# Performance work log

Measured on AMD Instinct MI355X. Metric: run time of the kernel, lower is better.

## Reference

```python
import jax, jax.numpy as jnp
import numpy as np

EPS = 1e-05
ITERS = 3


def safe_norm(s, axis):
    return jnp.sqrt(jnp.sum(s * s, axis=axis, keepdims=True) + EPS)


def squash(s, axis):
    norm = safe_norm(s, axis)
    return (norm / (1.0 + norm)) * s / norm


def setup_inputs() -> dict:
    key = jax.random.key(0)
    k1, k2 = jax.random.split(key)
    b, B, C, P, h, w = 4, 288, 32, 16, 14, 14  # B = K*K*32, P = pose 4x4
    u = jax.random.normal(k1, (b, B, C, P, h, w), dtype=jnp.float32)
    a = jax.random.uniform(k2, (b, B, h, w), dtype=jnp.float32)
    return {"u": u, "a": a}


def reference(u, a):
    # mode='dynamic': activation a is unused by this routing variant.
    # max_min_norm over pose axis (3), max/min over input-capsule axis (1)
    norm = safe_norm(u, 3)                          # (b,B,C,1,h,w)
    max_n = jnp.max(norm, axis=1, keepdims=True)    # (b,1,C,1,h,w)
    min_n = jnp.min(norm, axis=1, keepdims=True)
    u = u / (max_n - min_n)

    b, B, C, P, h, w = u.shape
    r = jnp.zeros((b, B, C, 1, h, w), dtype=u.dtype)
    v = None
    for i in range(ITERS):
        c = jax.nn.softmax(r, axis=2)                               # over C
        v = squash(jnp.sum(c * u, axis=1, keepdims=True), 3)        # (b,1,C,P,h,w)
        if i != ITERS - 1:
            r = r + jnp.sum(u * v, axis=3, keepdims=True)           # agreement
    a_out = safe_norm(v, 3)                                         # (b,1,C,1,h,w)
    return (jnp.squeeze(v, 1), jnp.squeeze(jnp.squeeze(a_out, 1), 2))
```

## Files before the change

### kernel.cpp

```cpp
#include <hip/hip_runtime.h>


constexpr int kB    = 4;
constexpr int kIC   = 288;
constexpr int kOC   = 32;
constexpr int kP    = 16;
constexpr int kHW   = 196;
constexpr int kNPOS = kB * kHW;
constexpr int kPAIR = 16;
constexpr int kNTILES = 25;
constexpr int kNCH  = 16;
constexpr int kBCH  = kIC / kNCH;
constexpr int kSCP  = kOC * kP * kNPOS;
constexpr int kSC   = kOC * kNPOS;
constexpr int kBStride2 = kOC * kP * kHW / 2;
constexpr int kNBLK = kNTILES * kNCH;
constexpr float kEPS = 1e-5f;

__device__ inline void decomp(int l, int& tile, int& chunk) {
    const int logical = (l & 7) * (kNBLK / 8) + (l >> 3);
    tile  = logical >> 4;
    chunk = logical & 15;
}

__global__ __launch_bounds__(512, 4) void pass1_kernel(
    const float* __restrict__ U, float* __restrict__ s0,
    unsigned int* __restrict__ maxb, unsigned int* __restrict__ minb)
{
    int tile, chunk;
    decomp(blockIdx.x, tile, chunk);
    const int tid = threadIdx.x;
    const int j   = tid & 15;
    const int c   = tid >> 4;
    int n0 = tile * 32 + 2 * j;
    const bool valid = (n0 < kNPOS);
    if (!valid) n0 = kNPOS - 2;
    const int b  = n0 / kHW;
    const int hw = n0 - b * kHW;
    const int B0 = chunk * kBCH;
    const float2* up = (const float2*)(U + (size_t)(((b * kIC + B0) * kOC + c) * kP) * kHW + hw);

    float2 sacc[kP];
#pragma unroll
    for (int p = 0; p < kP; ++p) sacc[p] = make_float2(0.f, 0.f);
    float2 mx = make_float2(0.f, 0.f);
    float2 mn = make_float2(3.4e38f, 3.4e38f);

    for (int Bi = 0; Bi < kBCH; ++Bi) {
        float2 u[kP];
#pragma unroll
        for (int p = 0; p < kP; ++p) u[p] = up[p * (kHW / 2)];
        float2 nsq = make_float2(kEPS, kEPS);
#pragma unroll
        for (int p = 0; p < kP; ++p) {
            nsq.x = fmaf(u[p].x, u[p].x, nsq.x);
            nsq.y = fmaf(u[p].y, u[p].y, nsq.y);
            sacc[p].x += u[p].x;
            sacc[p].y += u[p].y;
        }
        const float nrx = sqrtf(nsq.x), nry = sqrtf(nsq.y);
        mx.x = fmaxf(mx.x, nrx); mx.y = fmaxf(mx.y, nry);
        mn.x = fminf(mn.x, nrx); mn.y = fminf(mn.y, nry);
        up += kBStride2;
    }
    if (valid) {
        const int cn = c * kNPOS + n0;
        atomicMax(&maxb[cn],     __float_as_uint(mx.x));
        atomicMax(&maxb[cn + 1], __float_as_uint(mx.y));
        atomicMin(&minb[cn],     __float_as_uint(mn.x));
        atomicMin(&minb[cn + 1], __float_as_uint(mn.y));
#pragma unroll
        for (int p = 0; p < kP; ++p) {
            atomicAdd(&s0[(c * kP + p) * kNPOS + n0],     sacc[p].x);
            atomicAdd(&s0[(c * kP + p) * kNPOS + n0 + 1], sacc[p].y);
        }
    }
}

__global__ void v0_kernel(float* __restrict__ s0,
                          const unsigned int* __restrict__ maxb,
                          const unsigned int* __restrict__ minb,
                          float* __restrict__ scaleb)
{
    const int i = blockIdx.x * blockDim.x + threadIdx.x;
    if (i >= kSC) return;
    const int c = i / kNPOS;
    const int n = i - c * kNPOS;
    const float mx = __uint_as_float(maxb[i]);
    const float mn = __uint_as_float(minb[i]);
    const float sc = 1.f / (mx - mn);
    scaleb[i] = sc;
    float sv[kP];
    float nsq = kEPS;
#pragma unroll
    for (int p = 0; p < kP; ++p) {
        const float v = s0[(c * kP + p) * kNPOS + n] * sc * (1.f / 32.f);
        sv[p] = v;
        nsq = fmaf(v, v, nsq);
    }
    const float inv = 1.f / (1.f + sqrtf(nsq));
#pragma unroll
    for (int p = 0; p < kP; ++p)
        s0[(c * kP + p) * kNPOS + n] = sv[p] * inv;
}

__global__ __launch_bounds__(512, 3) void route_kernel(
    const float* __restrict__ U, const float* __restrict__ Vr,
    const float* __restrict__ scaleb, float* __restrict__ sout)
{
    __shared__ float2 ldsM[8 * kPAIR];
    __shared__ float2 ldsS[8 * kPAIR];
    int tile, chunk;
    decomp(blockIdx.x, tile, chunk);
    const int tid = threadIdx.x;
    const int j   = tid & 15;
    const int c   = tid >> 4;
    const int wv  = tid >> 6;
    int n0 = tile * 32 + 2 * j;
    const bool valid = (n0 < kNPOS);
    if (!valid) n0 = kNPOS - 2;
    const int b  = n0 / kHW;
    const int hw = n0 - b * kHW;
    const int B0 = chunk * kBCH;
    const float2* up = (const float2*)(U + (size_t)(((b * kIC + B0) * kOC + c) * kP) * kHW + hw);

    float2 vr[kP];
#pragma unroll
    for (int p = 0; p < kP; ++p)
        vr[p] = *(const float2*)&Vr[(c * kP + p) * kNPOS + n0];
    const float2 sc = *(const float2*)&scaleb[c * kNPOS + n0];

    float2 acc[kP];
#pragma unroll
    for (int p = 0; p < kP; ++p) acc[p] = make_float2(0.f, 0.f);

    for (int Bi = 0; Bi < kBCH; ++Bi) {
        float2 u[kP];
#pragma unroll
        for (int p = 0; p < kP; ++p) u[p] = up[p * (kHW / 2)];
        float2 d = make_float2(0.f, 0.f);
#pragma unroll
        for (int p = 0; p < kP; ++p) {
            d.x = fmaf(u[p].x, vr[p].x, d.x);
            d.y = fmaf(u[p].y, vr[p].y, d.y);
        }
        float2 r = make_float2(sc.x * d.x, sc.y * d.y);

        float2 m = r;
        m.x = fmaxf(m.x, __shfl_xor(m.x, 16)); m.y = fmaxf(m.y, __shfl_xor(m.y, 16));
        m.x = fmaxf(m.x, __shfl_xor(m.x, 32)); m.y = fmaxf(m.y, __shfl_xor(m.y, 32));
        if ((tid & 63) < kPAIR) ldsM[wv * kPAIR + j] = m;
        __syncthreads();
        float2 mxv = ldsM[j];
#pragma unroll
        for (int w = 1; w < 8; ++w) {
            const float2 t = ldsM[w * kPAIR + j];
            mxv.x = fmaxf(mxv.x, t.x); mxv.y = fmaxf(mxv.y, t.y);
        }
        const float2 e = make_float2(__expf(r.x - mxv.x), __expf(r.y - mxv.y));
        float2 z = e;
        z.x += __shfl_xor(z.x, 16); z.y += __shfl_xor(z.y, 16);
        z.x += __shfl_xor(z.x, 32); z.y += __shfl_xor(z.y, 32);
        if ((tid & 63) < kPAIR) ldsS[wv * kPAIR + j] = z;
        __syncthreads();
        float2 Z = ldsS[j];
#pragma unroll
        for (int w = 1; w < 8; ++w) {
            const float2 t = ldsS[w * kPAIR + j];
            Z.x += t.x; Z.y += t.y;
        }
        const float2 cb = make_float2(e.x / Z.x, e.y / Z.y);
#pragma unroll
        for (int p = 0; p < kP; ++p) {
            acc[p].x = fmaf(cb.x, u[p].x, acc[p].x);
            acc[p].y = fmaf(cb.y, u[p].y, acc[p].y);
        }
        up += kBStride2;
    }
    if (valid) {
#pragma unroll
        for (int p = 0; p < kP; ++p) {
            atomicAdd(&sout[(c * kP + p) * kNPOS + n0],     sc.x * acc[p].x);
            atomicAdd(&sout[(c * kP + p) * kNPOS + n0 + 1], sc.y * acc[p].y);
        }
    }
}

__global__ void v1_kernel(float* __restrict__ v0buf,
                          const float* __restrict__ s1)
{
    const int i = blockIdx.x * blockDim.x + threadIdx.x;
    if (i >= kSC) return;
    const int c = i / kNPOS;
    const int n = i - c * kNPOS;
    float sv[kP];
    float nsq = kEPS;
#pragma unroll
    for (int p = 0; p < kP; ++p) {
        const float v = s1[(c * kP + p) * kNPOS + n];
        sv[p] = v;
        nsq = fmaf(v, v, nsq);
    }
    const float inv = 1.f / (1.f + sqrtf(nsq));
#pragma unroll
    for (int p = 0; p < kP; ++p)
        v0buf[(c * kP + p) * kNPOS + n] += sv[p] * inv;
}

__global__ void final_kernel(const float* __restrict__ s2, float* __restrict__ out)
{
    const int i = blockIdx.x * blockDim.x + threadIdx.x;
    if (i >= kSC) return;
    const int c = i / kNPOS;
    const int n = i - c * kNPOS;
    const int b = n / kHW;
    const int hw = n - b * kHW;
    float sv[kP];
    float nsq = kEPS;
#pragma unroll
    for (int p = 0; p < kP; ++p) {
        const float v = s2[(c * kP + p) * kNPOS + n];
        sv[p] = v;
        nsq = fmaf(v, v, nsq);
    }
    const float inv = 1.f / (1.f + sqrtf(nsq));
    float vs = 0.f;
#pragma unroll
    for (int p = 0; p < kP; ++p) {
        const float v = sv[p] * inv;
        out[(size_t)((b * kOC + c) * kP + p) * kHW + hw] = v;
        vs = fmaf(v, v, vs);
    }
    out[(size_t)kSCP + (b * kOC + c) * kHW + hw] = sqrtf(vs + kEPS);
}

extern "C" void kernel_launch(void* const* d_in, const int* in_sizes, int n_in,
                              void* d_out, int out_size, void* d_ws, size_t ws_size,
                              hipStream_t stream) {
    const float* U = (const float*)d_in[0];
    float* out = (float*)d_out;
    float* ws  = (float*)d_ws;

    float* s0 = ws;
    float* s1 = ws + kSCP;
    float* s2 = ws + 2 * kSCP;
    unsigned int* maxb = (unsigned int*)(ws + 3 * kSCP);
    unsigned int* minb = maxb + kSC;
    float* scaleb = (float*)(minb + kSC);

    hipMemsetAsync(s0, 0, (size_t)3 * kSCP * sizeof(float), stream);
    hipMemsetAsync(maxb, 0, (size_t)kSC * sizeof(unsigned int), stream);
    hipMemsetAsync(minb, 0x7F, (size_t)kSC * sizeof(unsigned int), stream);

    pass1_kernel<<<kNBLK, 512, 0, stream>>>(U, s0, maxb, minb);
    v0_kernel<<<(kSC + 255) / 256, 256, 0, stream>>>(s0, maxb, minb, scaleb);
    route_kernel<<<kNBLK, 512, 0, stream>>>(U, s0, scaleb, s1);
    v1_kernel<<<(kSC + 255) / 256, 256, 0, stream>>>(s0, s1);
    route_kernel<<<kNBLK, 512, 0, stream>>>(U, s0, scaleb, s2);
    final_kernel<<<(kSC + 255) / 256, 256, 0, stream>>>(s2, out);
}
```

Measured before the change: 1.048 ms.

## Cache bf16 relayouted copy of U in pass1 for route kernels

Pass1 now writes a bf16-rounded copy of the input capsules, packed per tile and chunk into a contiguous slab layout. Both routing passes read this packed copy instead of re-reading fp32 U with strided access. This halves the bytes read by the routing passes and makes those loads contiguous, at the cost of an extra write in pass1 and bf16 precision in the agreement and weighted sums.

Result: faster. 953.9 us (-8.9%).

```diff
diff --git a/kernel.cpp b/kernel.cpp
--- a/kernel.cpp
+++ b/kernel.cpp
@@ -1,20 +1,20 @@
 #include <hip/hip_runtime.h>
 
 
-constexpr int kB    = 4;
 constexpr int kIC   = 288;
 constexpr int kOC   = 32;
 constexpr int kP    = 16;
 constexpr int kHW   = 196;
-constexpr int kNPOS = kB * kHW;
-constexpr int kPAIR = 16;
-constexpr int kNTILES = 25;
+constexpr int kNPOS = 4 * kHW;
+constexpr int kNT   = 25;
 constexpr int kNCH  = 16;
 constexpr int kBCH  = kIC / kNCH;
 constexpr int kSCP  = kOC * kP * kNPOS;
 constexpr int kSC   = kOC * kNPOS;
-constexpr int kBStride2 = kOC * kP * kHW / 2;
-constexpr int kNBLK = kNTILES * kNCH;
+constexpr int kNBLK = kNT * kNCH;
+constexpr int kUB   = kOC * kP * kHW;
+constexpr int kRslab = kBCH * 8 * kOC * 16;
+constexpr size_t kRBytes = (size_t)kNBLK * kRslab * 8;
 constexpr float kEPS = 1e-5f;
 
 __device__ inline void decomp(int l, int& tile, int& chunk) {
@@ -23,8 +23,13 @@
     chunk = logical & 15;
 }
 
+__device__ inline unsigned bf16rne(float x) {
+    const unsigned u = __float_as_uint(x);
+    return (u + 0x7FFFu + ((u >> 16) & 1u)) >> 16;
+}
+
 __global__ __launch_bounds__(512, 4) void pass1_kernel(
-    const float* __restrict__ U, float* __restrict__ s0,
+    const float* __restrict__ U, uint2* __restrict__ R, float* __restrict__ s0,
     unsigned int* __restrict__ maxb, unsigned int* __restrict__ minb)
 {
     int tile, chunk;
@@ -38,7 +43,8 @@
     const int b  = n0 / kHW;
     const int hw = n0 - b * kHW;
     const int B0 = chunk * kBCH;
-    const float2* up = (const float2*)(U + (size_t)(((b * kIC + B0) * kOC + c) * kP) * kHW + hw);
+    const float* up = U + (size_t)(((b * kIC + B0) * kOC + c) * kP) * kHW + hw;
+    uint2* Rp = R + (size_t)(tile * kNCH + chunk) * kRslab + c * 16 + j;
 
     float2 sacc[kP];
 #pragma unroll
@@ -47,21 +53,23 @@
     float2 mn = make_float2(3.4e38f, 3.4e38f);
 
     for (int Bi = 0; Bi < kBCH; ++Bi) {
-        float2 u[kP];
-#pragma unroll
-        for (int p = 0; p < kP; ++p) u[p] = up[p * (kHW / 2)];
         float2 nsq = make_float2(kEPS, kEPS);
 #pragma unroll
-        for (int p = 0; p < kP; ++p) {
-            nsq.x = fmaf(u[p].x, u[p].x, nsq.x);
-            nsq.y = fmaf(u[p].y, u[p].y, nsq.y);
-            sacc[p].x += u[p].x;
-            sacc[p].y += u[p].y;
+        for (int p2 = 0; p2 < 8; ++p2) {
+            const float2 a0 = *(const float2*)(up + (2 * p2)     * kHW);
+            const float2 a1 = *(const float2*)(up + (2 * p2 + 1) * kHW);
+            nsq.x = fmaf(a0.x, a0.x, nsq.x); nsq.y = fmaf(a0.y, a0.y, nsq.y);
+            nsq.x = fmaf(a1.x, a1.x, nsq.x); nsq.y = fmaf(a1.y, a1.y, nsq.y);
+            sacc[2 * p2].x     += a0.x; sacc[2 * p2].y     += a0.y;
+            sacc[2 * p2 + 1].x += a1.x; sacc[2 * p2 + 1].y += a1.y;
+            Rp[(Bi * 8 + p2) * (kOC * 16)] =
+                make_uint2(bf16rne(a0.x) | (bf16rne(a0.y) << 16),
+                           bf16rne(a1.x) | (bf16rne(a1.y) << 16));
         }
         const float nrx = sqrtf(nsq.x), nry = sqrtf(nsq.y);
         mx.x = fmaxf(mx.x, nrx); mx.y = fmaxf(mx.y, nry);
         mn.x = fminf(mn.x, nrx); mn.y = fminf(mn.y, nry);
-        up += kBStride2;
+        up += kUB;
     }
     if (valid) {
         const int cn = c * kNPOS + n0;
@@ -105,11 +113,11 @@
 }
 
 __global__ __launch_bounds__(512, 3) void route_kernel(
-    const float* __restrict__ U, const float* __restrict__ Vr,
+    const uint2* __restrict__ R, const float* __restrict__ Vr,
     const float* __restrict__ scaleb, float* __restrict__ sout)
 {
-    __shared__ float2 ldsM[8 * kPAIR];
-    __shared__ float2 ldsS[8 * kPAIR];
+    __shared__ float2 ldsM[8 * 16];
+    __shared__ float2 ldsS[8 * 16];
     int tile, chunk;
     decomp(blockIdx.x, tile, chunk);
     const int tid = threadIdx.x;
@@ -119,10 +127,7 @@
     int n0 = tile * 32 + 2 * j;
     const bool valid = (n0 < kNPOS);
     if (!valid) n0 = kNPOS - 2;
-    const int b  = n0 / kHW;
-    const int hw = n0 - b * kHW;
-    const int B0 = chunk * kBCH;
-    const float2* up = (const float2*)(U + (size_t)(((b * kIC + B0) * kOC + c) * kP) * kHW + hw);
+    const uint2* Rp = R + (size_t)(tile * kNCH + chunk) * kRslab + c * 16 + j;
 
     float2 vr[kP];
 #pragma unroll
@@ -137,7 +142,13 @@
     for (int Bi = 0; Bi < kBCH; ++Bi) {
         float2 u[kP];
 #pragma unroll
-        for (int p = 0; p < kP; ++p) u[p] = up[p * (kHW / 2)];
+        for (int p2 = 0; p2 < 8; ++p2) {
+            const uint2 w = Rp[(Bi * 8 + p2) * (kOC * 16)];
+            u[2 * p2].x     = __uint_as_float(w.x << 16);
+            u[2 * p2].y     = __uint_as_float(w.x & 0xFFFF0000u);
+            u[2 * p2 + 1].x = __uint_as_float(w.y << 16);
+            u[2 * p2 + 1].y = __uint_as_float(w.y & 0xFFFF0000u);
+        }
         float2 d = make_float2(0.f, 0.f);
 #pragma unroll
         for (int p = 0; p < kP; ++p) {
@@ -149,24 +160,24 @@
         float2 m = r;
         m.x = fmaxf(m.x, __shfl_xor(m.x, 16)); m.y = fmaxf(m.y, __shfl_xor(m.y, 16));
         m.x = fmaxf(m.x, __shfl_xor(m.x, 32)); m.y = fmaxf(m.y, __shfl_xor(m.y, 32));
-        if ((tid & 63) < kPAIR) ldsM[wv * kPAIR + j] = m;
+        if ((tid & 63) < 16) ldsM[wv * 16 + j] = m;
         __syncthreads();
         float2 mxv = ldsM[j];
 #pragma unroll
         for (int w = 1; w < 8; ++w) {
-            const float2 t = ldsM[w * kPAIR + j];
+            const float2 t = ldsM[w * 16 + j];
             mxv.x = fmaxf(mxv.x, t.x); mxv.y = fmaxf(mxv.y, t.y);
         }
         const float2 e = make_float2(__expf(r.x - mxv.x), __expf(r.y - mxv.y));
         float2 z = e;
         z.x += __shfl_xor(z.x, 16); z.y += __shfl_xor(z.y, 16);
         z.x += __shfl_xor(z.x, 32); z.y += __shfl_xor(z.y, 32);
-        if ((tid & 63) < kPAIR) ldsS[wv * kPAIR + j] = z;
+        if ((tid & 63) < 16) ldsS[wv * 16 + j] = z;
         __syncthreads();
         float2 Z = ldsS[j];
 #pragma unroll
         for (int w = 1; w < 8; ++w) {
-            const float2 t = ldsS[w * kPAIR + j];
+            const float2 t = ldsS[w * 16 + j];
             Z.x += t.x; Z.y += t.y;
         }
         const float2 cb = make_float2(e.x / Z.x, e.y / Z.y);
@@ -175,7 +186,6 @@
             acc[p].x = fmaf(cb.x, u[p].x, acc[p].x);
             acc[p].y = fmaf(cb.y, u[p].y, acc[p].y);
         }
-        up += kBStride2;
     }
     if (valid) {
 #pragma unroll
@@ -239,12 +249,13 @@
                               hipStream_t stream) {
     const float* U = (const float*)d_in[0];
     float* out = (float*)d_out;
-    float* ws  = (float*)d_ws;
-
-    float* s0 = ws;
-    float* s1 = ws + kSCP;
-    float* s2 = ws + 2 * kSCP;
-    unsigned int* maxb = (unsigned int*)(ws + 3 * kSCP);
+    char* wsb  = (char*)d_ws;
+
+    uint2* R   = (uint2*)wsb;
+    float* s0  = (float*)(wsb + kRBytes);
+    float* s1  = s0 + kSCP;
+    float* s2  = s1 + kSCP;
+    unsigned int* maxb = (unsigned int*)(s2 + kSCP);
     unsigned int* minb = maxb + kSC;
     float* scaleb = (float*)(minb + kSC);
 
@@ -252,10 +263,10 @@
     hipMemsetAsync(maxb, 0, (size_t)kSC * sizeof(unsigned int), stream);
     hipMemsetAsync(minb, 0x7F, (size_t)kSC * sizeof(unsigned int), stream);
 
-    pass1_kernel<<<kNBLK, 512, 0, stream>>>(U, s0, maxb, minb);
+    pass1_kernel<<<kNBLK, 512, 0, stream>>>(U, R, s0, maxb, minb);
     v0_kernel<<<(kSC + 255) / 256, 256, 0, stream>>>(s0, maxb, minb, scaleb);
-    route_kernel<<<kNBLK, 512, 0, stream>>>(U, s0, scaleb, s1);
+    route_kernel<<<kNBLK, 512, 0, stream>>>(R, s0, scaleb, s1);
     v1_kernel<<<(kSC + 255) / 256, 256, 0, stream>>>(s0, s1);
-    route_kernel<<<kNBLK, 512, 0, stream>>>(U, s0, scaleb, s2);
+    route_kernel<<<kNBLK, 512, 0, stream>>>(R, s0, scaleb, s2);
     final_kernel<<<(kSC + 255) / 256, 256, 0, stream>>>(s2, out);
 }
```
